# Kernel tuning notes

Hardware: AMD Instinct MI355X
Metric: run time of the kernel (lower is better)

The kernel has to match this reference:

```python
import jax, jax.numpy as jnp
import numpy as np
from jax import lax

WINDOW_SIZE = 11
SIGMA = 1.5
CHANNEL = 1
C1 = 0.01 ** 2
C2 = 0.03 ** 2


def _make_window(window_size: int, channel: int) -> jnp.ndarray:
    x = np.arange(window_size, dtype=np.float32)
    g = np.exp(-((x - window_size // 2) ** 2) / (2.0 * SIGMA ** 2)).astype(np.float32)
    g = g / g.sum()
    w3 = g[:, None, None] * g[None, :, None] * g[None, None, :]  # [k,k,k]
    # depthwise kernel, OIDHW with I=1, O=channel
    w = np.broadcast_to(w3[None, None], (channel, 1, window_size, window_size, window_size))
    return jnp.asarray(np.ascontiguousarray(w), dtype=jnp.float32)


def _conv3d(x, window, channel):
    pad = WINDOW_SIZE // 2
    return lax.conv_general_dilated(
        x, window,
        window_strides=(1, 1, 1),
        padding=[(pad, pad)] * 3,
        dimension_numbers=('NCDHW', 'OIDHW', 'NCDHW'),
        feature_group_count=channel,
    )


def setup_inputs() -> dict:
    key = jax.random.key(0)
    k1, k2 = jax.random.split(key)
    shape = (2, 1, 128, 256, 256)
    img1 = jax.random.uniform(k1, shape, dtype=jnp.float32)
    img2 = jax.random.uniform(k2, shape, dtype=jnp.float32)
    window = _make_window(WINDOW_SIZE, CHANNEL)
    return {"img1": img1, "img2": img2, "window": window}


def reference(img1, img2, window):
    channel = img1.shape[1]
    conv = lambda x: _conv3d(x, window, channel)
    mu1 = conv(img1)
    mu2 = conv(img2)
    mu1_sq = mu1 * mu1
    mu2_sq = mu2 * mu2
    mu1_mu2 = mu1 * mu2
    sigma1_sq = conv(img1 * img1) - mu1_sq
    sigma2_sq = conv(img2 * img2) - mu2_sq
    sigma12 = conv(img1 * img2) - mu1_mu2
    ssim_map = ((2 * mu1_mu2 + C1) * (2 * sigma12 + C2)) / ((mu1_sq + mu2_sq + C1) * (sigma1_sq + sigma2_sq + C2))
    return 1.0 - jnp.mean(ssim_map)
```

## Files before the change

kernel.cpp:

```cpp
#include <hip/hip_runtime.h>


#define DD 128
#define HH 256
#define WW 256
#define TH 32
#define TW 16
#define DC 32
#define KS 11
#define HALO 5
#define XH 42
#define XW 26
#define XSTR 28
#define WBSTR 17
#define WBPL (XH * WBSTR)
#define NTH 512
#define NPTS (XH * XW)
#define PLANE 65536
#define C1F 1.0e-4f
#define C2F 9.0e-4f
#define NVOX (2.0 * 128.0 * 256.0 * 256.0)

__global__ void ssim_init_kernel(const float* __restrict__ win,
                                 double* __restrict__ acc,
                                 float* __restrict__ g) {
    int i = threadIdx.x;
    if (i == 0) acc[0] = 0.0;
    if (i < KS) {
        float s = 0.f;
        #pragma unroll 1
        for (int j = 0; j < KS * KS; ++j) s += win[i * KS * KS + j];
        g[i] = s;
    }
}

__global__ __launch_bounds__(NTH, 4)
void ssim_main_kernel(const float* __restrict__ img1,
                      const float* __restrict__ img2,
                      const float* __restrict__ gcoef,
                      double* __restrict__ acc) {
    __shared__ float xt[XH * XSTR];
    __shared__ float yt[XH * XSTR];
    __shared__ float wb[5 * WBPL];
    __shared__ double red[NTH / 64];

    const int tid = threadIdx.x;
    const int tx = tid & 15;
    const int ty = tid >> 4;
    const int w0 = blockIdx.x * TW;
    const int h0 = blockIdx.y * TH;
    const int b  = blockIdx.z >> 2;
    const int d0 = (blockIdx.z & 3) * DC;

    const float* base1 = img1 + (size_t)b * (DD * PLANE);
    const float* base2 = img2 + (size_t)b * (DD * PLANE);

    int   goff[3];
    int   loff[3];
    float mskf[3];
    #pragma unroll
    for (int sg = 0; sg < 3; ++sg) {
        int p = tid + sg * NTH;
        int r = p / XW;
        int c = p - r * XW;
        int gh = h0 - HALO + r;
        int gw = w0 - HALO + c;
        bool v = (p < NPTS) && ((unsigned)gh < HH) && ((unsigned)gw < WW);
        goff[sg] = v ? (gh * WW + gw) : 0;
        mskf[sg] = v ? 1.f : 0.f;
        loff[sg] = r * XSTR + c;
    }

    float G[KS];
    #pragma unroll
    for (int i = 0; i < KS; ++i) G[i] = gcoef[i];

    float ring[5][KS];
    #pragma unroll
    for (int f = 0; f < 5; ++f)
        #pragma unroll
        for (int i = 0; i < KS; ++i) ring[f][i] = 0.f;

    float pv1[3], pv2[3];
    {
        int dIn = d0 - HALO;
        if ((unsigned)dIn < DD) {
            const float* s1 = base1 + dIn * PLANE;
            const float* s2 = base2 + dIn * PLANE;
            #pragma unroll
            for (int sg = 0; sg < 3; ++sg) {
                pv1[sg] = s1[goff[sg]];
                pv2[sg] = s2[goff[sg]];
            }
        } else {
            #pragma unroll
            for (int sg = 0; sg < 3; ++sg) { pv1[sg] = 0.f; pv2[sg] = 0.f; }
        }
    }

    double lsum = 0.0;

    for (int s = 0; s < DC + 2 * HALO; ++s) {
        #pragma unroll
        for (int f = 0; f < 5; ++f)
            #pragma unroll
            for (int i = 0; i < KS - 1; ++i) ring[f][i] = ring[f][i + 1];

        #pragma unroll
        for (int sg = 0; sg < 3; ++sg) {
            int p = tid + sg * NTH;
            if (p < NPTS) {
                xt[loff[sg]] = pv1[sg] * mskf[sg];
                yt[loff[sg]] = pv2[sg] * mskf[sg];
            }
        }
        __syncthreads();

        {
            int dIn = d0 - HALO + s + 1;
            if ((s + 1 < DC + 2 * HALO) && ((unsigned)dIn < DD)) {
                const float* s1 = base1 + dIn * PLANE;
                const float* s2 = base2 + dIn * PLANE;
                #pragma unroll
                for (int sg = 0; sg < 3; ++sg) {
                    pv1[sg] = s1[goff[sg]];
                    pv2[sg] = s2[goff[sg]];
                }
            } else {
                #pragma unroll
                for (int sg = 0; sg < 3; ++sg) { pv1[sg] = 0.f; pv2[sg] = 0.f; }
            }
        }

        {
            const float* xrow = &xt[ty * XSTR + tx];
            const float* yrow = &yt[ty * XSTR + tx];
            float a0 = 0.f, a1 = 0.f, a2 = 0.f, a3 = 0.f, a4 = 0.f;
            #pragma unroll
            for (int k = 0; k < KS; ++k) {
                float xv = xrow[k], yv = yrow[k], gk = G[k];
                float txv = gk * xv, tyv = gk * yv;
                a0 += txv; a1 += tyv;
                a2 += txv * xv; a3 += tyv * yv; a4 += txv * yv;
            }
            int o = ty * WBSTR + tx;
            wb[o] = a0; wb[WBPL + o] = a1; wb[2 * WBPL + o] = a2;
            wb[3 * WBPL + o] = a3; wb[4 * WBPL + o] = a4;
        }
        if (tid < (XH * TW - NTH)) {
            int r = TH + ty;
            const float* xrow = &xt[r * XSTR + tx];
            const float* yrow = &yt[r * XSTR + tx];
            float a0 = 0.f, a1 = 0.f, a2 = 0.f, a3 = 0.f, a4 = 0.f;
            #pragma unroll
            for (int k = 0; k < KS; ++k) {
                float xv = xrow[k], yv = yrow[k], gk = G[k];
                float txv = gk * xv, tyv = gk * yv;
                a0 += txv; a1 += tyv;
                a2 += txv * xv; a3 += tyv * yv; a4 += txv * yv;
            }
            int o = r * WBSTR + tx;
            wb[o] = a0; wb[WBPL + o] = a1; wb[2 * WBPL + o] = a2;
            wb[3 * WBPL + o] = a3; wb[4 * WBPL + o] = a4;
        }
        __syncthreads();

        float s0 = 0.f, s1 = 0.f, s2 = 0.f, s3 = 0.f, s4 = 0.f;
        #pragma unroll
        for (int k = 0; k < KS; ++k) {
            int o = (ty + k) * WBSTR + tx;
            float gk = G[k];
            s0 += gk * wb[o];
            s1 += gk * wb[WBPL + o];
            s2 += gk * wb[2 * WBPL + o];
            s3 += gk * wb[3 * WBPL + o];
            s4 += gk * wb[4 * WBPL + o];
        }
        ring[0][KS-1] = s0; ring[1][KS-1] = s1; ring[2][KS-1] = s2;
        ring[3][KS-1] = s3; ring[4][KS-1] = s4;

        if (s >= 2 * HALO) {
            float m1 = 0.f, m2 = 0.f, exx = 0.f, eyy = 0.f, exy = 0.f;
            #pragma unroll
            for (int i = 0; i < KS; ++i) {
                float gi = G[i];
                m1  += gi * ring[0][i];
                m2  += gi * ring[1][i];
                exx += gi * ring[2][i];
                eyy += gi * ring[3][i];
                exy += gi * ring[4][i];
            }
            float mu11 = m1 * m1, mu22 = m2 * m2, mu12 = m1 * m2;
            float sg1  = exx - mu11;
            float sg2  = eyy - mu22;
            float sg12 = exy - mu12;
            float num = (2.f * mu12 + C1F) * (2.f * sg12 + C2F);
            float den = (mu11 + mu22 + C1F) * (sg1 + sg2 + C2F);
            lsum += (double)(num / den);
        }
    }

    #pragma unroll
    for (int off = 32; off > 0; off >>= 1)
        lsum += __shfl_down(lsum, off, 64);
    int lane = tid & 63, wid = tid >> 6;
    if (lane == 0) red[wid] = lsum;
    __syncthreads();
    if (tid == 0) {
        double bsum = 0.0;
        #pragma unroll
        for (int wv = 0; wv < NTH / 64; ++wv) bsum += red[wv];
        atomicAdd(acc, bsum);
    }
}

__global__ void ssim_fin_kernel(const double* __restrict__ acc,
                                float* __restrict__ out) {
    out[0] = (float)(1.0 - acc[0] / NVOX);
}

extern "C" void kernel_launch(void* const* d_in, const int* in_sizes, int n_in,
                              void* d_out, int out_size, void* d_ws, size_t ws_size,
                              hipStream_t stream) {
    const float* img1 = (const float*)d_in[0];
    const float* img2 = (const float*)d_in[1];
    const float* win  = (const float*)d_in[2];
    double* acc = (double*)d_ws;
    float*  g   = (float*)((char*)d_ws + 16);

    hipLaunchKernelGGL(ssim_init_kernel, dim3(1), dim3(64), 0, stream, win, acc, g);
    hipLaunchKernelGGL(ssim_main_kernel, dim3(WW / TW, HH / TH, 2 * (DD / DC)),
                       dim3(NTH), 0, stream, img1, img2, g, acc);
    hipLaunchKernelGGL(ssim_fin_kernel, dim3(1), dim3(1), 0, stream, acc, (float*)d_out);
}
```

Measured before the change: 398.6 us.

## Vectorize slice loads and register-block the W and H convolution passes

Slice staging now uses one float4 global load per thread, with a 32-wide aligned halo instead of scalar loads at 26 columns. The W-pass computes 4 outputs per thread from float4 shared reads, cutting shared traffic through register reuse. The H-pass computes 2 rows per thread and writes to a new intermediate buffer in packed float4 layout. Only a fraction of threads work in each pass, which adds an extra barrier stage and leaves lanes idle.

```diff
diff --git a/kernel.cpp b/kernel.cpp
--- a/kernel.cpp
+++ b/kernel.cpp
@@ -7,15 +7,13 @@
 #define TH 32
 #define TW 16
 #define DC 32
+#define SLICES (DC + 10)
 #define KS 11
-#define HALO 5
 #define XH 42
-#define XW 26
-#define XSTR 28
-#define WBSTR 17
-#define WBPL (XH * WBSTR)
+#define XSTR 52
+#define WBAS 17
+#define WBBS 16
 #define NTH 512
-#define NPTS (XH * XW)
 #define PLANE 65536
 #define C1F 1.0e-4f
 #define C2F 9.0e-4f
@@ -39,9 +37,12 @@
                       const float* __restrict__ img2,
                       const float* __restrict__ gcoef,
                       double* __restrict__ acc) {
-    __shared__ float xt[XH * XSTR];
-    __shared__ float yt[XH * XSTR];
-    __shared__ float wb[5 * WBPL];
+    __shared__ __align__(16) float xt[XH * XSTR];
+    __shared__ __align__(16) float yt[XH * XSTR];
+    __shared__ float4 wbA[XH * WBAS];
+    __shared__ __align__(16) float wbB[XH * WBBS];
+    __shared__ float4 xfA[TH * TW];
+    __shared__ float  xfB[TH * TW];
     __shared__ double red[NTH / 64];
 
     const int tid = threadIdx.x;
@@ -55,21 +56,13 @@
     const float* base1 = img1 + (size_t)b * (DD * PLANE);
     const float* base2 = img2 + (size_t)b * (DD * PLANE);
 
-    int   goff[3];
-    int   loff[3];
-    float mskf[3];
-    #pragma unroll
-    for (int sg = 0; sg < 3; ++sg) {
-        int p = tid + sg * NTH;
-        int r = p / XW;
-        int c = p - r * XW;
-        int gh = h0 - HALO + r;
-        int gw = w0 - HALO + c;
-        bool v = (p < NPTS) && ((unsigned)gh < HH) && ((unsigned)gw < WW);
-        goff[sg] = v ? (gh * WW + gw) : 0;
-        mskf[sg] = v ? 1.f : 0.f;
-        loff[sg] = r * XSTR + c;
-    }
+    const int sr = tid >> 3;
+    const int sc = (tid & 7) << 2;
+    const int gh = h0 - 5 + sr;
+    const int gw = w0 - 8 + sc;
+    const bool sOk = (tid < 336) && ((unsigned)gh < HH) && ((unsigned)gw < WW);
+    const int gOfs = sOk ? (gh * WW + gw) : 0;
+    const int lOfs = sr * XSTR + sc;
 
     float G[KS];
     #pragma unroll
@@ -81,121 +74,141 @@
         #pragma unroll
         for (int i = 0; i < KS; ++i) ring[f][i] = 0.f;
 
-    float pv1[3], pv2[3];
+    const float4 z4 = make_float4(0.f, 0.f, 0.f, 0.f);
+    float4 pA = z4, pB = z4;
+
     {
-        int dIn = d0 - HALO;
-        if ((unsigned)dIn < DD) {
-            const float* s1 = base1 + dIn * PLANE;
-            const float* s2 = base2 + dIn * PLANE;
-            #pragma unroll
-            for (int sg = 0; sg < 3; ++sg) {
-                pv1[sg] = s1[goff[sg]];
-                pv2[sg] = s2[goff[sg]];
-            }
-        } else {
-            #pragma unroll
-            for (int sg = 0; sg < 3; ++sg) { pv1[sg] = 0.f; pv2[sg] = 0.f; }
-        }
-    }
+        int dIn = d0 - 5;
+        if (sOk && (unsigned)dIn < DD) {
+            pA = *(const float4*)(base1 + dIn * PLANE + gOfs);
+            pB = *(const float4*)(base2 + dIn * PLANE + gOfs);
+        }
+    }
+    if (tid < 336) {
+        *(float4*)&xt[lOfs] = pA;
+        *(float4*)&yt[lOfs] = pB;
+    }
+    {
+        int dIn = d0 - 4;
+        pA = z4; pB = z4;
+        if (sOk && (unsigned)dIn < DD) {
+            pA = *(const float4*)(base1 + dIn * PLANE + gOfs);
+            pB = *(const float4*)(base2 + dIn * PLANE + gOfs);
+        }
+    }
+    __syncthreads();
 
     double lsum = 0.0;
 
-    for (int s = 0; s < DC + 2 * HALO; ++s) {
+    for (int s = 0; s < SLICES; ++s) {
+        if (tid < 168) {
+            const int r = tid >> 2, q = tid & 3;
+            const float* xp = &xt[r * XSTR + (q << 2)];
+            const float* yp = &yt[r * XSTR + (q << 2)];
+            float a0[4] = {0,0,0,0}, a1[4] = {0,0,0,0}, a2[4] = {0,0,0,0},
+                  a3[4] = {0,0,0,0}, a4[4] = {0,0,0,0};
+            #pragma unroll
+            for (int bdx = 0; bdx < 5; ++bdx) {
+                float4 xv4 = *(const float4*)(xp + (bdx << 2));
+                float4 yv4 = *(const float4*)(yp + (bdx << 2));
+                #pragma unroll
+                for (int i = 0; i < 4; ++i) {
+                    const int c = bdx * 4 + i;
+                    if (c < 3 || c > 16) continue;
+                    const float xv = (i == 0) ? xv4.x : (i == 1) ? xv4.y : (i == 2) ? xv4.z : xv4.w;
+                    const float yv = (i == 0) ? yv4.x : (i == 1) ? yv4.y : (i == 2) ? yv4.z : yv4.w;
+                    #pragma unroll
+                    for (int j = 0; j < 4; ++j) {
+                        const int k = c - 3 - j;
+                        if (k < 0 || k >= KS) continue;
+                        const float t1 = G[k] * xv;
+                        const float t2 = G[k] * yv;
+                        a0[j] += t1;
+                        a1[j] += t2;
+                        a2[j] = fmaf(t1, xv, a2[j]);
+                        a3[j] = fmaf(t2, yv, a3[j]);
+                        a4[j] = fmaf(t1, yv, a4[j]);
+                    }
+                }
+            }
+            #pragma unroll
+            for (int j = 0; j < 4; ++j)
+                wbA[r * WBAS + (q << 2) + j] = make_float4(a0[j], a1[j], a2[j], a3[j]);
+            *(float4*)&wbB[r * WBBS + (q << 2)] = make_float4(a4[0], a4[1], a4[2], a4[3]);
+        }
+        __syncthreads();
+
+        if (s + 1 < SLICES) {
+            if (tid < 336) {
+                *(float4*)&xt[lOfs] = pA;
+                *(float4*)&yt[lOfs] = pB;
+            }
+        }
+        {
+            int dIn = d0 - 3 + s;
+            pA = z4; pB = z4;
+            if (sOk && ((unsigned)dIn < DD) && (s + 2 < SLICES)) {
+                pA = *(const float4*)(base1 + dIn * PLANE + gOfs);
+                pB = *(const float4*)(base2 + dIn * PLANE + gOfs);
+            }
+        }
+        if (tid < 256) {
+            const int m2 = tid >> 4;
+            const int cx = tid & 15;
+            float b0 = 0.f, b1 = 0.f, b2 = 0.f, b3 = 0.f, b4 = 0.f;
+            float c0 = 0.f, c1 = 0.f, c2 = 0.f, c3 = 0.f, c4 = 0.f;
+            #pragma unroll
+            for (int j = 0; j < KS + 1; ++j) {
+                float4 A = wbA[(2 * m2 + j) * WBAS + cx];
+                float  B = wbB[(2 * m2 + j) * WBBS + cx];
+                if (j < KS) {
+                    const float gk = G[j];
+                    b0 = fmaf(gk, A.x, b0); b1 = fmaf(gk, A.y, b1);
+                    b2 = fmaf(gk, A.z, b2); b3 = fmaf(gk, A.w, b3);
+                    b4 = fmaf(gk, B,   b4);
+                }
+                if (j >= 1) {
+                    const float gk = G[j - 1];
+                    c0 = fmaf(gk, A.x, c0); c1 = fmaf(gk, A.y, c1);
+                    c2 = fmaf(gk, A.z, c2); c3 = fmaf(gk, A.w, c3);
+                    c4 = fmaf(gk, B,   c4);
+                }
+            }
+            const int o0 = (2 * m2) * TW + cx;
+            xfA[o0]      = make_float4(b0, b1, b2, b3);
+            xfB[o0]      = b4;
+            xfA[o0 + TW] = make_float4(c0, c1, c2, c3);
+            xfB[o0 + TW] = c4;
+        }
+        __syncthreads();
+
         #pragma unroll
         for (int f = 0; f < 5; ++f)
             #pragma unroll
             for (int i = 0; i < KS - 1; ++i) ring[f][i] = ring[f][i + 1];
-
-        #pragma unroll
-        for (int sg = 0; sg < 3; ++sg) {
-            int p = tid + sg * NTH;
-            if (p < NPTS) {
-                xt[loff[sg]] = pv1[sg] * mskf[sg];
-                yt[loff[sg]] = pv2[sg] * mskf[sg];
-            }
-        }
-        __syncthreads();
-
         {
-            int dIn = d0 - HALO + s + 1;
-            if ((s + 1 < DC + 2 * HALO) && ((unsigned)dIn < DD)) {
-                const float* s1 = base1 + dIn * PLANE;
-                const float* s2 = base2 + dIn * PLANE;
-                #pragma unroll
-                for (int sg = 0; sg < 3; ++sg) {
-                    pv1[sg] = s1[goff[sg]];
-                    pv2[sg] = s2[goff[sg]];
-                }
-            } else {
-                #pragma unroll
-                for (int sg = 0; sg < 3; ++sg) { pv1[sg] = 0.f; pv2[sg] = 0.f; }
-            }
-        }
-
-        {
-            const float* xrow = &xt[ty * XSTR + tx];
-            const float* yrow = &yt[ty * XSTR + tx];
-            float a0 = 0.f, a1 = 0.f, a2 = 0.f, a3 = 0.f, a4 = 0.f;
-            #pragma unroll
-            for (int k = 0; k < KS; ++k) {
-                float xv = xrow[k], yv = yrow[k], gk = G[k];
-                float txv = gk * xv, tyv = gk * yv;
-                a0 += txv; a1 += tyv;
-                a2 += txv * xv; a3 += tyv * yv; a4 += txv * yv;
-            }
-            int o = ty * WBSTR + tx;
-            wb[o] = a0; wb[WBPL + o] = a1; wb[2 * WBPL + o] = a2;
-            wb[3 * WBPL + o] = a3; wb[4 * WBPL + o] = a4;
-        }
-        if (tid < (XH * TW - NTH)) {
-            int r = TH + ty;
-            const float* xrow = &xt[r * XSTR + tx];
-            const float* yrow = &yt[r * XSTR + tx];
-            float a0 = 0.f, a1 = 0.f, a2 = 0.f, a3 = 0.f, a4 = 0.f;
-            #pragma unroll
-            for (int k = 0; k < KS; ++k) {
-                float xv = xrow[k], yv = yrow[k], gk = G[k];
-                float txv = gk * xv, tyv = gk * yv;
-                a0 += txv; a1 += tyv;
-                a2 += txv * xv; a3 += tyv * yv; a4 += txv * yv;
-            }
-            int o = r * WBSTR + tx;
-            wb[o] = a0; wb[WBPL + o] = a1; wb[2 * WBPL + o] = a2;
-            wb[3 * WBPL + o] = a3; wb[4 * WBPL + o] = a4;
-        }
-        __syncthreads();
-
-        float s0 = 0.f, s1 = 0.f, s2 = 0.f, s3 = 0.f, s4 = 0.f;
-        #pragma unroll
-        for (int k = 0; k < KS; ++k) {
-            int o = (ty + k) * WBSTR + tx;
-            float gk = G[k];
-            s0 += gk * wb[o];
-            s1 += gk * wb[WBPL + o];
-            s2 += gk * wb[2 * WBPL + o];
-            s3 += gk * wb[3 * WBPL + o];
-            s4 += gk * wb[4 * WBPL + o];
-        }
-        ring[0][KS-1] = s0; ring[1][KS-1] = s1; ring[2][KS-1] = s2;
-        ring[3][KS-1] = s3; ring[4][KS-1] = s4;
-
-        if (s >= 2 * HALO) {
+            const float4 S = xfA[ty * TW + tx];
+            const float s4v = xfB[ty * TW + tx];
+            ring[0][KS-1] = S.x; ring[1][KS-1] = S.y; ring[2][KS-1] = S.z;
+            ring[3][KS-1] = S.w; ring[4][KS-1] = s4v;
+        }
+        if (s >= 10) {
             float m1 = 0.f, m2 = 0.f, exx = 0.f, eyy = 0.f, exy = 0.f;
             #pragma unroll
             for (int i = 0; i < KS; ++i) {
-                float gi = G[i];
-                m1  += gi * ring[0][i];
-                m2  += gi * ring[1][i];
-                exx += gi * ring[2][i];
-                eyy += gi * ring[3][i];
-                exy += gi * ring[4][i];
-            }
-            float mu11 = m1 * m1, mu22 = m2 * m2, mu12 = m1 * m2;
-            float sg1  = exx - mu11;
-            float sg2  = eyy - mu22;
-            float sg12 = exy - mu12;
-            float num = (2.f * mu12 + C1F) * (2.f * sg12 + C2F);
-            float den = (mu11 + mu22 + C1F) * (sg1 + sg2 + C2F);
+                const float gi = G[i];
+                m1  = fmaf(gi, ring[0][i], m1);
+                m2  = fmaf(gi, ring[1][i], m2);
+                exx = fmaf(gi, ring[2][i], exx);
+                eyy = fmaf(gi, ring[3][i], eyy);
+                exy = fmaf(gi, ring[4][i], exy);
+            }
+            const float mu11 = m1 * m1, mu22 = m2 * m2, mu12 = m1 * m2;
+            const float sg1  = exx - mu11;
+            const float sg2  = eyy - mu22;
+            const float sg12 = exy - mu12;
+            const float num = (2.f * mu12 + C1F) * (2.f * sg12 + C2F);
+            const float den = (mu11 + mu22 + C1F) * (sg1 + sg2 + C2F);
             lsum += (double)(num / den);
         }
     }
@@ -203,7 +216,7 @@
     #pragma unroll
     for (int off = 32; off > 0; off >>= 1)
         lsum += __shfl_down(lsum, off, 64);
-    int lane = tid & 63, wid = tid >> 6;
+    const int lane = tid & 63, wid = tid >> 6;
     if (lane == 0) red[wid] = lsum;
     __syncthreads();
     if (tid == 0) {
```

New measurement: 762.6 us. +91.3%, slower.
